# Kernel tuning notes

Hardware: AMD Instinct MI355X
Metric: run time of the kernel (lower is better)

Reference implementation:

```python
import jax, jax.numpy as jnp
import numpy as np

N = 50000
E = 1600000
F_IN = 3
C = 40

def _linear_params(key, fan_in, fan_out):
    k1, k2 = jax.random.split(key)
    bound = 1.0 / np.sqrt(fan_in)
    W = jax.random.uniform(k1, (fan_in, fan_out), jnp.float32, -bound, bound)
    b = jax.random.uniform(k2, (fan_out,), jnp.float32, -bound, bound)
    return W, b

def setup_inputs() -> dict:
    key = jax.random.key(0)
    ks = jax.random.split(key, 9)
    x = jax.random.normal(ks[0], (N, F_IN), jnp.float32)
    pos = jax.random.normal(ks[1], (N, 3), jnp.float32)
    edge_index = jax.random.randint(ks[2], (2, E), 0, N, jnp.int64)
    W1, b1 = _linear_params(ks[3], F_IN + 3, 64)   # local_nn layer 1
    W2, b2 = _linear_params(ks[4], 64, 64)          # local_nn layer 2
    W3, b3 = _linear_params(ks[5], 64, 128)         # global_nn layer 1
    W4, b4 = _linear_params(ks[6], 128, 1024)       # global_nn layer 2
    W5, b5 = _linear_params(ks[7], 1024, 64)        # global_nn layer 3
    Wf, bf = _linear_params(ks[8], 64, C)           # fc
    return {"x": x, "pos": pos, "edge_index": edge_index,
            "W1": W1, "b1": b1, "W2": W2, "b2": b2,
            "W3": W3, "b3": b3, "W4": W4, "b4": b4,
            "W5": W5, "b5": b5, "Wf": Wf, "bf": bf}

def reference(x, pos, edge_index, W1, b1, W2, b2, W3, b3, W4, b4, W5, b5, Wf, bf):
    # PyG PointNetConv: add self-loops by default
    loop = jnp.arange(N, dtype=edge_index.dtype)
    src = jnp.concatenate([edge_index[0], loop])  # j
    dst = jnp.concatenate([edge_index[1], loop])  # i
    # message: local_nn(concat(x_j, pos_j - pos_i))  -> [E+N, 64]
    msg_in = jnp.concatenate([x[src], pos[src] - pos[dst]], axis=1)
    h = jax.nn.relu(msg_in @ W1 + b1)
    h = h @ W2 + b2
    # max-aggregate to destination nodes
    agg = jax.ops.segment_max(h, dst, num_segments=N)
    # global_nn
    g = jax.nn.relu(agg @ W3 + b3)
    g = jax.nn.relu(g @ W4 + b4)
    g = g @ W5 + b5
    # trailing relu + fc + log_softmax
    out = jax.nn.relu(g) @ Wf + bf
    return jax.nn.log_softmax(out, axis=1)
```

## Files before the change

### kernel.cpp

```cpp
#include <hip/hip_runtime.h>
#include <cstddef>
#include <cmath>

typedef __attribute__((ext_vector_type(8))) short bf16x8;
typedef __attribute__((ext_vector_type(4))) float f32x4;

static __device__ __forceinline__ f32x4 mfma16(bf16x8 a, bf16x8 b, f32x4 c) {
    return __builtin_amdgcn_mfma_f32_16x16x32_bf16(a, b, c, 0, 0, 0);
}
static __device__ __forceinline__ unsigned short f2bf(float f) {
    unsigned int u = __float_as_uint(f);
    return (unsigned short)((u + 0x7FFFu + ((u >> 16) & 1u)) >> 16);
}

#define NBK 256
#define CAP 12288

__global__ __launch_bounds__(256) void k_bin(const int* __restrict__ ei, int E,
                                             unsigned int* __restrict__ gcur,
                                             unsigned int* __restrict__ pairs) {
    __shared__ unsigned int h[NBK];
    __shared__ unsigned int base[NBK];
    int tid = threadIdx.x;
    h[tid] = 0u;
    __syncthreads();
    int idx = blockIdx.x * 256 + tid;
    int e0 = idx * 4;
    unsigned int vals[4]; int bs[4]; unsigned int rk[4]; int cnt4 = 0;
    if (e0 + 3 < E) {
        int4 s = ((const int4*)ei)[idx];
        int4 d = ((const int4*)(ei + E))[idx];
        int sa[4] = {s.x, s.y, s.z, s.w};
        int da[4] = {d.x, d.y, d.z, d.w};
        cnt4 = 4;
#pragma unroll
        for (int j = 0; j < 4; ++j) {
            bs[j] = da[j] >> 8;
            vals[j] = (unsigned int)sa[j] | ((unsigned int)(da[j] & 255) << 16);
            rk[j] = atomicAdd(&h[bs[j]], 1u);
        }
    } else {
        for (int e = e0; e < E; ++e) {
            int j = cnt4++;
            int sv = ei[e], dv = ei[E + e];
            bs[j] = dv >> 8;
            vals[j] = (unsigned int)sv | ((unsigned int)(dv & 255) << 16);
            rk[j] = atomicAdd(&h[bs[j]], 1u);
        }
    }
    __syncthreads();
    unsigned int c = h[tid];
    base[tid] = c ? atomicAdd(&gcur[tid], c) : 0u;
    __syncthreads();
    for (int j = 0; j < cnt4; ++j) {
        unsigned int p = base[bs[j]] + rk[j];
        if (p < CAP) pairs[(size_t)bs[j] * CAP + p] = vals[j];
    }
}

__global__ __launch_bounds__(256) void k_build(const unsigned int* __restrict__ gcur,
                                               const unsigned int* __restrict__ pairs,
                                               unsigned int* __restrict__ list,
                                               unsigned int* __restrict__ off,
                                               unsigned int* __restrict__ deg, int N) {
    __shared__ unsigned int cntL[NBK];
    __shared__ unsigned int s[NBK];
    __shared__ unsigned int curL[NBK];
    int b = blockIdx.x, t = threadIdx.x;
    unsigned int gstart = (unsigned int)b * CAP;
    unsigned int m = min(gcur[b], (unsigned int)CAP);
    cntL[t] = 0u;
    __syncthreads();
    for (unsigned int i = t; i < m; i += 256u)
        atomicAdd(&cntL[(pairs[gstart + i] >> 16) & 255u], 1u);
    __syncthreads();
    unsigned int c = cntL[t];
    s[t] = c;
    __syncthreads();
    for (int d = 1; d < 256; d <<= 1) {
        unsigned int v = (t >= d) ? s[t - d] : 0u;
        __syncthreads();
        s[t] += v;
        __syncthreads();
    }
    unsigned int excl = s[t] - c;
    int dst = b * 256 + t;
    if (dst < N) { off[dst] = gstart + excl; deg[dst] = c; }
    curL[t] = excl;
    __syncthreads();
    for (unsigned int i = t; i < m; i += 256u) {
        unsigned int v = pairs[gstart + i];
        unsigned int p = atomicAdd(&curL[(v >> 16) & 255u], 1u);
        list[gstart + p] = v & 0xFFFFu;
    }
}

__global__ void k_convert(const float* __restrict__ W1, const float* __restrict__ W2,
                          const float* __restrict__ W3, const float* __restrict__ W4,
                          const float* __restrict__ W5,
                          unsigned short* __restrict__ W1bt, unsigned short* __restrict__ W2bt,
                          unsigned short* __restrict__ W3bt, unsigned short* __restrict__ W4bt,
                          unsigned short* __restrict__ W5ct) {
    int id = blockIdx.x * 256 + threadIdx.x;
    if (id < 2048) {
        int n = id >> 5, k = id & 31;
        W1bt[id] = (k < 6) ? f2bf(W1[k * 64 + n]) : (unsigned short)0;
    } else if (id < 2048 + 4096) {
        int t = id - 2048;
        int n = t >> 6, k = t & 63;
        W2bt[t] = f2bf(W2[k * 64 + n]);
    } else if (id < 6144 + 8192) {
        int t = id - 6144;
        int n = t >> 6, k = t & 63;
        W3bt[t] = f2bf(W3[k * 128 + n]);
    } else if (id < 14336 + 131072) {
        int t = id - 14336;
        int n = t >> 7, k = t & 127;
        W4bt[t] = f2bf(W4[k * 1024 + n]);
    } else if (id < 145408 + 65536) {
        int t = id - 145408;
        int ch = t >> 12, rem = t & 4095;
        int n = rem >> 6, kl = rem & 63;
        W5ct[t] = f2bf(W5[(ch * 64 + kl) * 64 + n]);
    }
}

#define TPB_E 256
#define EDGE_WPB 4
__global__ __launch_bounds__(TPB_E, 4) void edge_kernel(
    const float* __restrict__ x, const float* __restrict__ pos,
    const unsigned int* __restrict__ off, const unsigned int* __restrict__ deg,
    const unsigned int* __restrict__ list,
    const unsigned short* __restrict__ W1bt, const float* __restrict__ b1,
    const unsigned short* __restrict__ W2bt, const float* __restrict__ b2,
    float* __restrict__ agg, int N, int dstStride)
{
    __shared__ __align__(16) short Hs[4][16 * 72];

    int tid = threadIdx.x;
    int lane = tid & 63;
    int w = tid >> 6;
    int lm = lane & 15;
    int quad = lane >> 4;
    short* H = Hs[w];
    int dst0 = blockIdx.x * EDGE_WPB + w;

    bf16x8 B1f[4], B2f[4][2];
    float b1c[4], b2c[4];
#pragma unroll
    for (int nt = 0; nt < 4; ++nt) {
        B1f[nt] = *(const bf16x8*)&W1bt[(nt * 16 + lm) * 32 + quad * 8];
        B2f[nt][0] = *(const bf16x8*)&W2bt[(nt * 16 + lm) * 64 + quad * 8];
        B2f[nt][1] = *(const bf16x8*)&W2bt[(nt * 16 + lm) * 64 + 32 + quad * 8];
        b1c[nt] = b1[nt * 16 + lm];
        b2c[nt] = b2[nt * 16 + lm];
    }

    unsigned int o0P = 0u, dgP = 0u;
    if (dst0 < N) { o0P = off[dst0]; dgP = deg[dst0]; }

    for (int dst = dst0; dst < N; dst += dstStride) {
        unsigned int o0 = o0P;
        int ecnt = (int)dgP;
        int dn = dst + dstStride;
        if (dn < N) { o0P = off[dn]; dgP = deg[dn]; }

        int M = ecnt + 1;
        float pi0 = pos[dst * 3 + 0], pi1 = pos[dst * 3 + 1], pi2 = pos[dst * 3 + 2];

        float m0 = -INFINITY, m1 = -INFINITY, m2 = -INFINITY, m3 = -INFINITY;

        auto ldidx = [&](int base) -> int {
            int i = min(base + lm, M - 1);
            return (i == 0) ? dst : (int)list[o0 + i - 1];
        };

        float vx0 = 0.f, vx1 = 0.f, vx2 = 0.f, vq0 = 0.f, vq1 = 0.f, vq2 = 0.f;
        int sNext = dst;
        if (quad == 0) {
            int s0 = ldidx(0);
            vx0 = x[s0 * 3 + 0]; vx1 = x[s0 * 3 + 1]; vx2 = x[s0 * 3 + 2];
            vq0 = pos[s0 * 3 + 0]; vq1 = pos[s0 * 3 + 1]; vq2 = pos[s0 * 3 + 2];
            if (16 < M) sNext = ldidx(16);
        }

        for (int base = 0; base < M; base += 16) {
            float nx0 = vx0, nx1 = vx1, nx2 = vx2, nq0 = vq0, nq1 = vq1, nq2 = vq2;
            int sN2 = sNext;
            if (quad == 0) {
                nx0 = x[sNext * 3 + 0]; nx1 = x[sNext * 3 + 1]; nx2 = x[sNext * 3 + 2];
                nq0 = pos[sNext * 3 + 0]; nq1 = pos[sNext * 3 + 1]; nq2 = pos[sNext * 3 + 2];
                if (base + 32 < M) sN2 = ldidx(base + 32);
            }
            bf16x8 A = {0, 0, 0, 0, 0, 0, 0, 0};
            if (quad == 0) {
                A[0] = (short)f2bf(vx0);
                A[1] = (short)f2bf(vx1);
                A[2] = (short)f2bf(vx2);
                A[3] = (short)f2bf(vq0 - pi0);
                A[4] = (short)f2bf(vq1 - pi1);
                A[5] = (short)f2bf(vq2 - pi2);
            }
#pragma unroll
            for (int nt = 0; nt < 4; ++nt) {
                f32x4 c = {0.f, 0.f, 0.f, 0.f};
                c = mfma16(A, B1f[nt], c);
#pragma unroll
                for (int r = 0; r < 4; ++r) {
                    float v = fmaxf(c[r] + b1c[nt], 0.f);
                    H[(quad * 4 + r) * 72 + nt * 16 + lm] = (short)f2bf(v);
                }
            }
            bf16x8 A2a = *(const bf16x8*)&H[lm * 72 + quad * 8];
            bf16x8 A2b = *(const bf16x8*)&H[lm * 72 + 32 + quad * 8];
            {
                f32x4 c = {0.f, 0.f, 0.f, 0.f};
                c = mfma16(A2a, B2f[0][0], c); c = mfma16(A2b, B2f[0][1], c);
                m0 = fmaxf(m0, fmaxf(fmaxf(c[0], c[1]), fmaxf(c[2], c[3])));
            }
            {
                f32x4 c = {0.f, 0.f, 0.f, 0.f};
                c = mfma16(A2a, B2f[1][0], c); c = mfma16(A2b, B2f[1][1], c);
                m1 = fmaxf(m1, fmaxf(fmaxf(c[0], c[1]), fmaxf(c[2], c[3])));
            }
            {
                f32x4 c = {0.f, 0.f, 0.f, 0.f};
                c = mfma16(A2a, B2f[2][0], c); c = mfma16(A2b, B2f[2][1], c);
                m2 = fmaxf(m2, fmaxf(fmaxf(c[0], c[1]), fmaxf(c[2], c[3])));
            }
            {
                f32x4 c = {0.f, 0.f, 0.f, 0.f};
                c = mfma16(A2a, B2f[3][0], c); c = mfma16(A2b, B2f[3][1], c);
                m3 = fmaxf(m3, fmaxf(fmaxf(c[0], c[1]), fmaxf(c[2], c[3])));
            }
            vx0 = nx0; vx1 = nx1; vx2 = nx2; vq0 = nq0; vq1 = nq1; vq2 = nq2;
            sNext = sN2;
        }

        m0 = fmaxf(m0, __shfl_xor(m0, 16, 64)); m0 = fmaxf(m0, __shfl_xor(m0, 32, 64));
        m1 = fmaxf(m1, __shfl_xor(m1, 16, 64)); m1 = fmaxf(m1, __shfl_xor(m1, 32, 64));
        m2 = fmaxf(m2, __shfl_xor(m2, 16, 64)); m2 = fmaxf(m2, __shfl_xor(m2, 32, 64));
        m3 = fmaxf(m3, __shfl_xor(m3, 16, 64)); m3 = fmaxf(m3, __shfl_xor(m3, 32, 64));

        float mv = (quad == 0) ? m0 : (quad == 1) ? m1 : (quad == 2) ? m2 : m3;
        agg[(size_t)dst * 64 + lane] = mv + b2c[quad];
    }
}

#define NNODE 64
__global__ __launch_bounds__(256, 2) void node_kernel(
    const float* __restrict__ agg,
    const unsigned short* __restrict__ W3bt, const float* __restrict__ b3,
    const unsigned short* __restrict__ W4bt, const float* __restrict__ b4,
    const unsigned short* __restrict__ W5ct, const float* __restrict__ b5,
    const float* __restrict__ Wf, const float* __restrict__ bf,
    float* __restrict__ out, int N)
{
    __shared__ __align__(16) char smem[79872];
    short* G1s = (short*)smem;
    float* G3f = (float*)smem;
    short* G2s = (short*)(smem + 17408);
    short* Wb4 = (short*)(smem + 26624);
    short* Wb5 = (short*)(smem + 61440);
    float* os  = (float*)(smem + 26624);

    int tid = threadIdx.x;
    int lane = tid & 63;
    int wm = tid >> 6;
    int lm = lane & 15;
    int quad = lane >> 4;
    int n0 = blockIdx.x * NNODE;

    auto stage = [&](int ch, int buf) {
        const unsigned short* g4 = W4bt + (size_t)ch * 8192;
        short* d4 = Wb4 + buf * 8704;
#pragma unroll
        for (int it = 0; it < 4; ++it) {
            int v = tid + it * 256;
            *(int4*)&d4[(v >> 4) * 136 + (v & 15) * 8] = *(const int4*)(g4 + v * 8);
        }
        const unsigned short* g5 = W5ct + (size_t)ch * 4096;
        short* d5 = Wb5 + buf * 4608;
#pragma unroll
        for (int it = 0; it < 2; ++it) {
            int v = tid + it * 256;
            *(int4*)&d5[(v >> 3) * 72 + (v & 7) * 8] = *(const int4*)(g5 + v * 8);
        }
    };

    stage(0, 0);

    {
        int arow = min(n0 + wm * 16 + lm, N - 1);
        bf16x8 A3[2];
#pragma unroll
        for (int f = 0; f < 2; ++f) {
            const float* p = agg + (size_t)arow * 64 + f * 32 + quad * 8;
            float4 u = *(const float4*)p;
            float4 v = *(const float4*)(p + 4);
            bf16x8 t;
            t[0] = (short)f2bf(u.x); t[1] = (short)f2bf(u.y);
            t[2] = (short)f2bf(u.z); t[3] = (short)f2bf(u.w);
            t[4] = (short)f2bf(v.x); t[5] = (short)f2bf(v.y);
            t[6] = (short)f2bf(v.z); t[7] = (short)f2bf(v.w);
            A3[f] = t;
        }
#pragma unroll
        for (int nt = 0; nt < 8; ++nt) {
            const unsigned short* wb = W3bt + (nt * 16 + lm) * 64 + quad * 8;
            f32x4 c = {0.f, 0.f, 0.f, 0.f};
            c = mfma16(A3[0], *(const bf16x8*)wb, c);
            c = mfma16(A3[1], *(const bf16x8*)(wb + 32), c);
            float bias = b3[nt * 16 + lm];
#pragma unroll
            for (int r = 0; r < 4; ++r) {
                float v = fmaxf(c[r] + bias, 0.f);
                G1s[(wm * 16 + quad * 4 + r) * 136 + nt * 16 + lm] = (short)f2bf(v);
            }
        }
    }

    bf16x8 A4[4];
#pragma unroll
    for (int f = 0; f < 4; ++f)
        A4[f] = *(const bf16x8*)&G1s[(wm * 16 + lm) * 136 + f * 32 + quad * 8];

    f32x4 acc3[4];
#pragma unroll
    for (int nt = 0; nt < 4; ++nt) {
        float b = b5[nt * 16 + lm];
        acc3[nt][0] = b; acc3[nt][1] = b; acc3[nt][2] = b; acc3[nt][3] = b;
    }

    __syncthreads();

    for (int ch = 0; ch < 16; ++ch) {
        int buf = ch & 1;
        if (ch < 15) stage(ch + 1, buf ^ 1);

        const short* w4b = Wb4 + buf * 8704;
        const short* w5b = Wb5 + buf * 4608;

#pragma unroll
        for (int nt = 0; nt < 4; ++nt) {
            const short* wb = w4b + (nt * 16 + lm) * 136 + quad * 8;
            f32x4 c = {0.f, 0.f, 0.f, 0.f};
            c = mfma16(A4[0], *(const bf16x8*)wb, c);
            c = mfma16(A4[1], *(const bf16x8*)(wb + 32), c);
            c = mfma16(A4[2], *(const bf16x8*)(wb + 64), c);
            c = mfma16(A4[3], *(const bf16x8*)(wb + 96), c);
            float bias = b4[ch * 64 + nt * 16 + lm];
#pragma unroll
            for (int r = 0; r < 4; ++r) {
                float v = fmaxf(c[r] + bias, 0.f);
                G2s[(wm * 16 + quad * 4 + r) * 72 + nt * 16 + lm] = (short)f2bf(v);
            }
        }
        bf16x8 A5_0 = *(const bf16x8*)&G2s[(wm * 16 + lm) * 72 + quad * 8];
        bf16x8 A5_1 = *(const bf16x8*)&G2s[(wm * 16 + lm) * 72 + 32 + quad * 8];
#pragma unroll
        for (int nt = 0; nt < 4; ++nt) {
            const short* wb = w5b + (nt * 16 + lm) * 72 + quad * 8;
            acc3[nt] = mfma16(A5_0, *(const bf16x8*)wb, acc3[nt]);
            acc3[nt] = mfma16(A5_1, *(const bf16x8*)(wb + 32), acc3[nt]);
        }
        __syncthreads();
    }

#pragma unroll
    for (int nt = 0; nt < 4; ++nt)
#pragma unroll
        for (int r = 0; r < 4; ++r)
            G3f[(wm * 16 + quad * 4 + r) * 68 + nt * 16 + lm] = fmaxf(acc3[nt][r], 0.f);
    __syncthreads();

    for (int idx = tid; idx < NNODE * 40; idx += 256) {
        int ln = idx / 40;
        int c = idx - ln * 40;
        float o = bf[c];
#pragma unroll 4
        for (int j = 0; j < 64; ++j)
            o = fmaf(G3f[ln * 68 + j], Wf[j * 40 + c], o);
        os[ln * 41 + c] = o;
    }
    __syncthreads();

    if (tid < NNODE && n0 + tid < N) {
        int ln = tid;
        float mx = os[ln * 41 + 0];
#pragma unroll
        for (int c = 1; c < 40; ++c) mx = fmaxf(mx, os[ln * 41 + c]);
        float s = 0.f;
#pragma unroll
        for (int c = 0; c < 40; ++c) s += expf(os[ln * 41 + c] - mx);
        float ls = logf(s) + mx;
        float* op = out + (size_t)(n0 + tid) * 40;
#pragma unroll
        for (int c = 0; c < 40; ++c) op[c] = os[ln * 41 + c] - ls;
    }
}

extern "C" void kernel_launch(void* const* d_in, const int* in_sizes, int n_in,
                              void* d_out, int out_size, void* d_ws, size_t ws_size,
                              hipStream_t stream) {
    const float* x   = (const float*)d_in[0];
    const float* pos = (const float*)d_in[1];
    const int*   ei  = (const int*)d_in[2];
    const float* W1  = (const float*)d_in[3];
    const float* b1  = (const float*)d_in[4];
    const float* W2  = (const float*)d_in[5];
    const float* b2  = (const float*)d_in[6];
    const float* W3  = (const float*)d_in[7];
    const float* b3  = (const float*)d_in[8];
    const float* W4  = (const float*)d_in[9];
    const float* b4  = (const float*)d_in[10];
    const float* W5  = (const float*)d_in[11];
    const float* b5  = (const float*)d_in[12];
    const float* Wf  = (const float*)d_in[13];
    const float* bf  = (const float*)d_in[14];
    float* out = (float*)d_out;

    int Nn = in_sizes[0] / 3;
    int E  = in_sizes[2] / 2;

    char* w = (char*)d_ws;
    size_t p = 0;
    auto take = [&](size_t bytes) { size_t q = p; p = (p + bytes + 255) & ~size_t(255); return (void*)(w + q); };
    unsigned int*   off   = (unsigned int*)take((size_t)Nn * 4);
    unsigned int*   deg   = (unsigned int*)take((size_t)Nn * 4);
    unsigned int*   gcur  = (unsigned int*)take(NBK * 4);
    unsigned int*   list  = (unsigned int*)take((size_t)NBK * CAP * 4);
    float*          agg   = (float*)take((size_t)Nn * 64 * 4);
    unsigned int*   pairs = (unsigned int*)agg;
    unsigned short* W1bt = (unsigned short*)take(2048 * 2);
    unsigned short* W2bt = (unsigned short*)take(4096 * 2);
    unsigned short* W3bt = (unsigned short*)take(8192 * 2);
    unsigned short* W4bt = (unsigned short*)take(131072 * 2);
    unsigned short* W5ct = (unsigned short*)take(65536 * 2);

    hipMemsetAsync(gcur, 0, NBK * 4, stream);
    k_convert<<<(2048 + 4096 + 8192 + 131072 + 65536 + 255) / 256, 256, 0, stream>>>(
        W1, W2, W3, W4, W5, W1bt, W2bt, W3bt, W4bt, W5ct);

    int q4 = (E + 3) / 4;
    int gb = (q4 + 255) / 256;
    k_bin<<<gb, 256, 0, stream>>>(ei, E, gcur, pairs);
    int nb = (Nn + 255) >> 8;
    k_build<<<nb, 256, 0, stream>>>(gcur, pairs, list, off, deg, Nn);

    int totalWaves = (Nn + 3) / 4;
    int eBlocks = (totalWaves + EDGE_WPB - 1) / EDGE_WPB;
    int dstStride = eBlocks * EDGE_WPB;
    edge_kernel<<<eBlocks, TPB_E, 0, stream>>>(
        x, pos, off, deg, list, W1bt, b1, W2bt, b2, agg, Nn, dstStride);

    node_kernel<<<(Nn + NNODE - 1) / NNODE, 256, 0, stream>>>(
        agg, W3bt, b3, W4bt, b4, W5ct, b5, Wf, bf, out, Nn);
}
```

Measured before the change: 318.0 us.

## Split node_kernel work across 8 waves with split-K reduction for W5

Doubles node_kernel to 512 threads, so each 16-row M tile is shared by two waves. The two waves split the N dimension of layers 3 and 4 and the K dimension of layer 5, and their partial W5 results are summed through shared memory before the relu. This gives more waves per block to hide latency and halves each wave's MFMA chain. In exchange it adds extra syncs and a shared-memory reduction, and the launch bound of 4 blocks of 512 threads per CU may be limited by the roughly 78KB of LDS each block uses.

Measured after the change: 303.5 us. 1.05x faster.

```diff
diff --git a/kernel.cpp b/kernel.cpp
--- a/kernel.cpp
+++ b/kernel.cpp
@@ -248,7 +248,7 @@
 }
 
 #define NNODE 64
-__global__ __launch_bounds__(256, 2) void node_kernel(
+__global__ __launch_bounds__(512, 4) void node_kernel(
     const float* __restrict__ agg,
     const unsigned short* __restrict__ W3bt, const float* __restrict__ b3,
     const unsigned short* __restrict__ W4bt, const float* __restrict__ b4,
@@ -267,6 +267,8 @@
     int tid = threadIdx.x;
     int lane = tid & 63;
     int wm = tid >> 6;
+    int m = wm & 3;
+    int h = wm >> 2;
     int lm = lane & 15;
     int quad = lane >> 4;
     int n0 = blockIdx.x * NNODE;
@@ -275,15 +277,14 @@
         const unsigned short* g4 = W4bt + (size_t)ch * 8192;
         short* d4 = Wb4 + buf * 8704;
 #pragma unroll
-        for (int it = 0; it < 4; ++it) {
-            int v = tid + it * 256;
+        for (int it = 0; it < 2; ++it) {
+            int v = tid + it * 512;
             *(int4*)&d4[(v >> 4) * 136 + (v & 15) * 8] = *(const int4*)(g4 + v * 8);
         }
         const unsigned short* g5 = W5ct + (size_t)ch * 4096;
         short* d5 = Wb5 + buf * 4608;
-#pragma unroll
-        for (int it = 0; it < 2; ++it) {
-            int v = tid + it * 256;
+        {
+            int v = tid;
             *(int4*)&d5[(v >> 3) * 72 + (v & 7) * 8] = *(const int4*)(g5 + v * 8);
         }
     };
@@ -291,7 +292,7 @@
     stage(0, 0);
 
     {
-        int arow = min(n0 + wm * 16 + lm, N - 1);
+        int arow = min(n0 + m * 16 + lm, N - 1);
         bf16x8 A3[2];
 #pragma unroll
         for (int f = 0; f < 2; ++f) {
@@ -306,7 +307,8 @@
             A3[f] = t;
         }
 #pragma unroll
-        for (int nt = 0; nt < 8; ++nt) {
+        for (int nt2 = 0; nt2 < 4; ++nt2) {
+            int nt = h * 4 + nt2;
             const unsigned short* wb = W3bt + (nt * 16 + lm) * 64 + quad * 8;
             f32x4 c = {0.f, 0.f, 0.f, 0.f};
             c = mfma16(A3[0], *(const bf16x8*)wb, c);
@@ -315,24 +317,24 @@
 #pragma unroll
             for (int r = 0; r < 4; ++r) {
                 float v = fmaxf(c[r] + bias, 0.f);
-                G1s[(wm * 16 + quad * 4 + r) * 136 + nt * 16 + lm] = (short)f2bf(v);
-            }
-        }
-    }
+                G1s[(m * 16 + quad * 4 + r) * 136 + nt * 16 + lm] = (short)f2bf(v);
+            }
+        }
+    }
+
+    f32x4 acc3[4];
+#pragma unroll
+    for (int nt = 0; nt < 4; ++nt) {
+        float b = (h == 0) ? b5[nt * 16 + lm] : 0.f;
+        acc3[nt][0] = b; acc3[nt][1] = b; acc3[nt][2] = b; acc3[nt][3] = b;
+    }
+
+    __syncthreads();
 
     bf16x8 A4[4];
 #pragma unroll
     for (int f = 0; f < 4; ++f)
-        A4[f] = *(const bf16x8*)&G1s[(wm * 16 + lm) * 136 + f * 32 + quad * 8];
-
-    f32x4 acc3[4];
-#pragma unroll
-    for (int nt = 0; nt < 4; ++nt) {
-        float b = b5[nt * 16 + lm];
-        acc3[nt][0] = b; acc3[nt][1] = b; acc3[nt][2] = b; acc3[nt][3] = b;
-    }
-
-    __syncthreads();
+        A4[f] = *(const bf16x8*)&G1s[(m * 16 + lm) * 136 + f * 32 + quad * 8];
 
     for (int ch = 0; ch < 16; ++ch) {
         int buf = ch & 1;
@@ -342,7 +344,8 @@
         const short* w5b = Wb5 + buf * 4608;
 
 #pragma unroll
-        for (int nt = 0; nt < 4; ++nt) {
+        for (int nt2 = 0; nt2 < 2; ++nt2) {
+            int nt = h * 2 + nt2;
             const short* wb = w4b + (nt * 16 + lm) * 136 + quad * 8;
             f32x4 c = {0.f, 0.f, 0.f, 0.f};
             c = mfma16(A4[0], *(const bf16x8*)wb, c);
@@ -353,28 +356,38 @@
 #pragma unroll
             for (int r = 0; r < 4; ++r) {
                 float v = fmaxf(c[r] + bias, 0.f);
-                G2s[(wm * 16 + quad * 4 + r) * 72 + nt * 16 + lm] = (short)f2bf(v);
-            }
-        }
-        bf16x8 A5_0 = *(const bf16x8*)&G2s[(wm * 16 + lm) * 72 + quad * 8];
-        bf16x8 A5_1 = *(const bf16x8*)&G2s[(wm * 16 + lm) * 72 + 32 + quad * 8];
+                G2s[(m * 16 + quad * 4 + r) * 72 + nt * 16 + lm] = (short)f2bf(v);
+            }
+        }
+        bf16x8 A5 = *(const bf16x8*)&G2s[(m * 16 + lm) * 72 + h * 32 + quad * 8];
 #pragma unroll
         for (int nt = 0; nt < 4; ++nt) {
-            const short* wb = w5b + (nt * 16 + lm) * 72 + quad * 8;
-            acc3[nt] = mfma16(A5_0, *(const bf16x8*)wb, acc3[nt]);
-            acc3[nt] = mfma16(A5_1, *(const bf16x8*)(wb + 32), acc3[nt]);
+            const short* wb = w5b + (nt * 16 + lm) * 72 + h * 32 + quad * 8;
+            acc3[nt] = mfma16(A5, *(const bf16x8*)wb, acc3[nt]);
         }
         __syncthreads();
     }
 
-#pragma unroll
-    for (int nt = 0; nt < 4; ++nt)
-#pragma unroll
-        for (int r = 0; r < 4; ++r)
-            G3f[(wm * 16 + quad * 4 + r) * 68 + nt * 16 + lm] = fmaxf(acc3[nt][r], 0.f);
-    __syncthreads();
-
-    for (int idx = tid; idx < NNODE * 40; idx += 256) {
+    if (h == 0) {
+#pragma unroll
+        for (int nt = 0; nt < 4; ++nt)
+#pragma unroll
+            for (int r = 0; r < 4; ++r)
+                G3f[(m * 16 + quad * 4 + r) * 68 + nt * 16 + lm] = acc3[nt][r];
+    }
+    __syncthreads();
+    if (h == 1) {
+#pragma unroll
+        for (int nt = 0; nt < 4; ++nt)
+#pragma unroll
+            for (int r = 0; r < 4; ++r) {
+                int idx = (m * 16 + quad * 4 + r) * 68 + nt * 16 + lm;
+                G3f[idx] = fmaxf(G3f[idx] + acc3[nt][r], 0.f);
+            }
+    }
+    __syncthreads();
+
+    for (int idx = tid; idx < NNODE * 40; idx += 512) {
         int ln = idx / 40;
         int c = idx - ln * 40;
         float o = bf[c];
@@ -454,6 +467,6 @@
     edge_kernel<<<eBlocks, TPB_E, 0, stream>>>(
         x, pos, off, deg, list, W1bt, b1, W2bt, b2, agg, Nn, dstStride);
 
-    node_kernel<<<(Nn + NNODE - 1) / NNODE, 256, 0, stream>>>(
+    node_kernel<<<(Nn + NNODE - 1) / NNODE, 512, 0, stream>>>(
         agg, W3bt, b3, W4bt, b4, W5ct, b5, Wf, bf, out, Nn);
 }
```
